# Performance work log

Hardware: AMD Instinct MI355X
Metric: run time of the kernel (lower is better)

The kernel has to match this reference:

```python
import jax, jax.numpy as jnp
import numpy as np
import math

H = 16
D_MODEL = 1024
D_K = D_MODEL // H
MAX_REL = 32
B, S = 2, 2048


def setup_inputs() -> dict:
    key = jax.random.key(0)
    ks = jax.random.split(key, 12)
    def w(k):
        return jax.random.normal(k, (D_MODEL, D_MODEL), jnp.float32) * 0.02
    def b(k):
        return jax.random.normal(k, (D_MODEL,), jnp.float32) * 0.02
    return {
        "query": jax.random.normal(ks[0], (B, S, D_MODEL), jnp.float32),
        "key": jax.random.normal(ks[1], (B, S, D_MODEL), jnp.float32),
        "value": jax.random.normal(ks[2], (B, S, D_MODEL), jnp.float32),
        "mask": jax.random.randint(ks[3], (B, S, S), 0, 2, jnp.int32),
        "Wq": w(ks[4]), "bq": b(ks[5]),
        "Wk": w(ks[6]), "bk": b(ks[7]),
        "Wv": w(ks[8]), "bv": b(ks[9]),
        "Wo": w(ks[10]), "bo": b(ks[11]),
        "rel_emb": jax.random.normal(jax.random.fold_in(key, 99), (2 * MAX_REL + 1, D_K), jnp.float32) * 0.02,
    }


def _rel_bias(q_len, k_len, rel_emb):
    # relative positions clamped to [-MAX_REL, MAX_REL], shifted to [0, 2*MAX_REL]
    rel = jnp.arange(q_len)[:, None] - jnp.arange(k_len)[None, :]
    rel = jnp.clip(rel, -MAX_REL, MAX_REL) + MAX_REL
    # embedding lookup then sum over d_k (torch code: permute(2,0,1).sum(0))
    return rel_emb[rel].sum(-1)  # [q_len, k_len], shared across heads/batch


def reference(query, key, value, mask, Wq, bq, Wk, bk, Wv, bv, Wo, bo, rel_emb):
    nb, qlen, _ = query.shape
    klen = key.shape[1]
    def proj(x, W, b):  # torch Linear: x @ W.T + b -> [B, L, H, D_K] -> [B, H, L, D_K]
        return (x @ W.T + b).reshape(nb, -1, H, D_K).transpose(0, 2, 1, 3)
    q = proj(query, Wq, bq)
    k = proj(key, Wk, bk)
    v = proj(value, Wv, bv)
    scores = jnp.einsum('bhqd,bhkd->bhqk', q, k) / math.sqrt(D_K)
    scores = scores + _rel_bias(qlen, klen, rel_emb)[None, None]
    scores = jnp.where(mask[:, None] == 0, -1e9, scores)
    p = jax.nn.softmax(scores, axis=-1)
    out = jnp.einsum('bhqk,bhkd->bhqd', p, v)
    out = out.transpose(0, 2, 1, 3).reshape(nb, -1, H * D_K)
    return out @ Wo.T + bo
```

## Files before the change

kernel.cpp:

```cpp
#include <hip/hip_runtime.h>
#include <hip/hip_bf16.h>
#include <stdint.h>
#include <math.h>

typedef __bf16 bf16;
typedef __attribute__((ext_vector_type(8))) __bf16 bf16x8;
typedef __attribute__((ext_vector_type(4))) float f32x4;

#define MFMA(a, b, c) __builtin_amdgcn_mfma_f32_16x16x32_bf16(a, b, c, 0, 0, 0)

__device__ __forceinline__ bf16x8 cvt8(const float* p) {
  f32x4 a = *(const f32x4*)p;
  f32x4 b = *(const f32x4*)(p + 4);
  bf16x8 o;
  o[0] = (bf16)a[0]; o[1] = (bf16)a[1]; o[2] = (bf16)a[2]; o[3] = (bf16)a[3];
  o[4] = (bf16)b[0]; o[5] = (bf16)b[1]; o[6] = (bf16)b[2]; o[7] = (bf16)b[3];
  return o;
}

__global__ __launch_bounds__(256) void pack_mask(const int* __restrict__ mask,
                                                 unsigned long long* __restrict__ pm,
                                                 int nwords) {
  const int lane = threadIdx.x & 63;
  const int wave = blockIdx.x * (blockDim.x >> 6) + (threadIdx.x >> 6);
  const int nwaves = gridDim.x * (blockDim.x >> 6);
  for (int w = wave; w < nwords; w += nwaves) {
    int m = mask[(size_t)w * 64 + lane];
    unsigned long long bits = __ballot(m != 0);
    if (lane == 0) pm[w] = bits;
  }
}

template <int SPLIT>
__global__ __launch_bounds__(256) void gemm_bt(const float* __restrict__ X,
                                               const float* __restrict__ W,
                                               const float* __restrict__ bias,
                                               void* __restrict__ out_) {
  __shared__ __align__(16) bf16 As[128 * 32];
  __shared__ __align__(16) bf16 Bs[128 * 32];
  const int tid = threadIdx.x, lane = tid & 63, w = tid >> 6;
  const int r16 = lane & 15, g4 = lane >> 4;
  const int m0 = blockIdx.x * 128, n0 = blockIdx.y * 128;

  f32x4 acc[4][4] = {};

  const int ra = tid >> 2;
  const int ca = (tid & 3) << 3;

  for (int k0 = 0; k0 < 1024; k0 += 32) {
    bf16x8 xa0 = cvt8(&X[(size_t)(m0 + ra) * 1024 + k0 + ca]);
    bf16x8 xa1 = cvt8(&X[(size_t)(m0 + 64 + ra) * 1024 + k0 + ca]);
    bf16x8 xb0 = cvt8(&W[(size_t)(n0 + ra) * 1024 + k0 + ca]);
    bf16x8 xb1 = cvt8(&W[(size_t)(n0 + 64 + ra) * 1024 + k0 + ca]);
    __syncthreads();
    *(bf16x8*)&As[ra * 32 + ca] = xa0;
    *(bf16x8*)&As[(ra + 64) * 32 + ca] = xa1;
    *(bf16x8*)&Bs[ra * 32 + ca] = xb0;
    *(bf16x8*)&Bs[(ra + 64) * 32 + ca] = xb1;
    __syncthreads();

    const int wm = (w >> 1) << 6, wn = (w & 1) << 6;
    bf16x8 af[4], bfr[4];
#pragma unroll
    for (int i = 0; i < 4; i++)
      af[i] = *(const bf16x8*)&As[(wm + i * 16 + r16) * 32 + g4 * 8];
#pragma unroll
    for (int j = 0; j < 4; j++)
      bfr[j] = *(const bf16x8*)&Bs[(wn + j * 16 + r16) * 32 + g4 * 8];
#pragma unroll
    for (int i = 0; i < 4; i++)
#pragma unroll
      for (int j = 0; j < 4; j++)
        acc[i][j] = MFMA(af[i], bfr[j], acc[i][j]);
  }

  const int wm = (w >> 1) << 6, wn = (w & 1) << 6;
#pragma unroll
  for (int j = 0; j < 4; j++) {
    const int col = n0 + wn + j * 16 + r16;
    const float bv = bias[col];
#pragma unroll
    for (int i = 0; i < 4; i++) {
      const int row0 = m0 + wm + i * 16 + g4 * 4;
#pragma unroll
      for (int r = 0; r < 4; r++) {
        float v = acc[i][j][r] + bv;
        const int row = row0 + r;
        if (SPLIT) {
          const int bb = row >> 11, s = row & 2047, h = col >> 6, d = col & 63;
          ((bf16*)out_)[((((size_t)bb * 16 + h) * 2048 + s) << 6) + d] = (bf16)v;
        } else {
          ((float*)out_)[(size_t)row * 1024 + col] = v;
        }
      }
    }
  }
}

__global__ __launch_bounds__(256) void attn_fwd(const bf16* __restrict__ Q,
                                                const bf16* __restrict__ Kb,
                                                const bf16* __restrict__ Vb,
                                                const unsigned long long* __restrict__ pm,
                                                const float* __restrict__ rel,
                                                bf16* __restrict__ ao) {
  constexpr int PAD = 72;
  __shared__ __align__(16) bf16 Ks[64 * PAD];
  __shared__ __align__(16) bf16 Vt[64 * PAD];
  __shared__ __align__(16) bf16 Ps[64 * PAD];
  __shared__ float rb[65];

  const int tid = threadIdx.x, lane = tid & 63, w = tid >> 6;
  const int r16 = lane & 15, g4 = lane >> 4;
  const int qt = blockIdx.x;
  const int bh = blockIdx.y;
  const int b = bh >> 4, h = bh & 15;

  const bf16* Qh = Q + (size_t)bh * 2048 * 64;
  const bf16* Kh = Kb + (size_t)bh * 2048 * 64;
  const bf16* Vh = Vb + (size_t)bh * 2048 * 64;

  if (tid < 65) {
    const float* e = rel + tid * 64;
    float s = 0.f;
#pragma unroll
    for (int i = 0; i < 64; i++) s += e[i];
    rb[tid] = s;
  }

  bf16x8 aq[2];
  {
    const int qrow = (qt << 6) + (w << 4) + r16;
    aq[0] = *(const bf16x8*)&Qh[(size_t)qrow * 64 + g4 * 8];
    aq[1] = *(const bf16x8*)&Qh[(size_t)qrow * 64 + 32 + g4 * 8];
  }

  f32x4 acc_o[4] = {};
  float mreg[4] = {-1e30f, -1e30f, -1e30f, -1e30f};
  float lreg[4] = {0.f, 0.f, 0.f, 0.f};

  __syncthreads();

  for (int t = 0; t < 32; t++) {
#pragma unroll
    for (int cc = 0; cc < 2; cc++) {
      const int c = tid + (cc << 8);
      const int key = c >> 3, f8 = (c & 7) << 3;
      bf16x8 kv = *(const bf16x8*)&Kh[(size_t)((t << 6) + key) * 64 + f8];
      *(bf16x8*)&Ks[key * PAD + f8] = kv;
      bf16x8 vv = *(const bf16x8*)&Vh[(size_t)((t << 6) + key) * 64 + f8];
#pragma unroll
      for (int j = 0; j < 8; j++) Vt[(f8 + j) * PAD + key] = vv[j];
    }
    __syncthreads();

    f32x4 sc[4];
#pragma unroll
    for (int f = 0; f < 4; f++) {
      f32x4 a = {};
#pragma unroll
      for (int kk = 0; kk < 2; kk++) {
        bf16x8 bk_ = *(const bf16x8*)&Ks[(f * 16 + r16) * PAD + kk * 32 + g4 * 8];
        a = MFMA(aq[kk], bk_, a);
      }
      sc[f] = a;
    }

    unsigned long long mw[4];
    const int qrow0 = (qt << 6) + (w << 4) + (g4 << 2);
#pragma unroll
    for (int r = 0; r < 4; r++)
      mw[r] = pm[(size_t)((b << 11) + qrow0 + r) * 32 + t];

    float s_[4][4];
#pragma unroll
    for (int f = 0; f < 4; f++) {
      const int kcol = (t << 6) + (f << 4) + r16;
#pragma unroll
      for (int r = 0; r < 4; r++) {
        int dd = (qrow0 + r) - kcol;
        dd = dd < -32 ? -32 : (dd > 32 ? 32 : dd);
        const bool on = (mw[r] >> ((f << 4) + r16)) & 1ull;
        float x = on ? sc[f][r] * 0.125f + rb[dd + 32] : -1e9f;
        s_[f][r] = (x == x) ? x : -1e9f;
      }
    }

    float rs[4];
#pragma unroll
    for (int r = 0; r < 4; r++) {
      float v = fmaxf(fmaxf(s_[0][r], s_[1][r]), fmaxf(s_[2][r], s_[3][r]));
#pragma unroll
      for (int d = 1; d < 16; d <<= 1) v = fmaxf(v, __shfl_xor(v, d, 16));
      const float mn = fmaxf(mreg[r], v);
      rs[r] = __expf(mreg[r] - mn);
      mreg[r] = mn;
    }
    float ps_[4] = {0.f, 0.f, 0.f, 0.f};
#pragma unroll
    for (int f = 0; f < 4; f++)
#pragma unroll
      for (int r = 0; r < 4; r++) {
        const float p = __expf(s_[f][r] - mreg[r]);
        ps_[r] += p;
        Ps[(w * 16 + g4 * 4 + r) * PAD + f * 16 + r16] = (bf16)p;
      }
#pragma unroll
    for (int r = 0; r < 4; r++) {
      float v = ps_[r];
#pragma unroll
      for (int d = 1; d < 16; d <<= 1) v += __shfl_xor(v, d, 16);
      lreg[r] = lreg[r] * rs[r] + v;
    }
#pragma unroll
    for (int f = 0; f < 4; f++)
#pragma unroll
      for (int r = 0; r < 4; r++) acc_o[f][r] *= rs[r];

#pragma unroll
    for (int kk = 0; kk < 2; kk++) {
      bf16x8 ap = *(const bf16x8*)&Ps[(w * 16 + r16) * PAD + kk * 32 + g4 * 8];
#pragma unroll
      for (int f = 0; f < 4; f++) {
        const int d = f * 16 + r16;
        bf16x8 bv_ = *(const bf16x8*)&Vt[d * PAD + kk * 32 + g4 * 8];
        acc_o[f] = MFMA(ap, bv_, acc_o[f]);
      }
    }
    __syncthreads();
  }

  const int qrow0 = (qt << 6) + (w << 4) + (g4 << 2);
#pragma unroll
  for (int r = 0; r < 4; r++) {
    const float inv = 1.f / lreg[r];
#pragma unroll
    for (int f = 0; f < 4; f++) {
      float v = acc_o[f][r] * inv;
      ao[(size_t)((b << 11) + qrow0 + r) * 1024 + (h << 6) + f * 16 + r16] = (bf16)v;
    }
  }
}

__global__ __launch_bounds__(256) void gemm_out(const bf16* __restrict__ X,
                                                const float* __restrict__ W,
                                                const float* __restrict__ bias,
                                                float* __restrict__ out) {
  __shared__ __align__(16) bf16 As[128 * 32];
  __shared__ __align__(16) bf16 Bs[128 * 32];
  const int tid = threadIdx.x, lane = tid & 63, w = tid >> 6;
  const int r16 = lane & 15, g4 = lane >> 4;
  const int m0 = blockIdx.x * 128, n0 = blockIdx.y * 128;

  f32x4 acc[4][4] = {};
  const int ra = tid >> 2;
  const int ca = (tid & 3) << 3;

  for (int k0 = 0; k0 < 1024; k0 += 32) {
    bf16x8 xa0 = *(const bf16x8*)&X[(size_t)(m0 + ra) * 1024 + k0 + ca];
    bf16x8 xa1 = *(const bf16x8*)&X[(size_t)(m0 + 64 + ra) * 1024 + k0 + ca];
    bf16x8 xb0 = cvt8(&W[(size_t)(n0 + ra) * 1024 + k0 + ca]);
    bf16x8 xb1 = cvt8(&W[(size_t)(n0 + 64 + ra) * 1024 + k0 + ca]);
    __syncthreads();
    *(bf16x8*)&As[ra * 32 + ca] = xa0;
    *(bf16x8*)&As[(ra + 64) * 32 + ca] = xa1;
    *(bf16x8*)&Bs[ra * 32 + ca] = xb0;
    *(bf16x8*)&Bs[(ra + 64) * 32 + ca] = xb1;
    __syncthreads();

    const int wm = (w >> 1) << 6, wn = (w & 1) << 6;
    bf16x8 af[4], bfr[4];
#pragma unroll
    for (int i = 0; i < 4; i++)
      af[i] = *(const bf16x8*)&As[(wm + i * 16 + r16) * 32 + g4 * 8];
#pragma unroll
    for (int j = 0; j < 4; j++)
      bfr[j] = *(const bf16x8*)&Bs[(wn + j * 16 + r16) * 32 + g4 * 8];
#pragma unroll
    for (int i = 0; i < 4; i++)
#pragma unroll
      for (int j = 0; j < 4; j++)
        acc[i][j] = MFMA(af[i], bfr[j], acc[i][j]);
  }

  const int wm = (w >> 1) << 6, wn = (w & 1) << 6;
#pragma unroll
  for (int j = 0; j < 4; j++) {
    const int col = n0 + wn + j * 16 + r16;
    const float bv = bias[col];
#pragma unroll
    for (int i = 0; i < 4; i++) {
      const int row0 = m0 + wm + i * 16 + g4 * 4;
#pragma unroll
      for (int r = 0; r < 4; r++)
        out[(size_t)(row0 + r) * 1024 + col] = acc[i][j][r] + bv;
    }
  }
}

extern "C" void kernel_launch(void* const* d_in, const int* in_sizes, int n_in,
                              void* d_out, int out_size, void* d_ws, size_t ws_size,
                              hipStream_t stream) {
  const float* query = (const float*)d_in[0];
  const float* key   = (const float*)d_in[1];
  const float* value = (const float*)d_in[2];
  const int*   mask  = (const int*)d_in[3];
  const float* Wq = (const float*)d_in[4];
  const float* bq = (const float*)d_in[5];
  const float* Wk = (const float*)d_in[6];
  const float* bk = (const float*)d_in[7];
  const float* Wv = (const float*)d_in[8];
  const float* bv = (const float*)d_in[9];
  const float* Wo = (const float*)d_in[10];
  const float* bo = (const float*)d_in[11];
  const float* rel = (const float*)d_in[12];

  char* ws = (char*)d_ws;
  bf16* Qb = (bf16*)ws;
  bf16* Kb = (bf16*)(ws + 8388608);
  bf16* Vb = (bf16*)(ws + 16777216);
  bf16* AO = (bf16*)(ws + 25165824);
  unsigned long long* PM = (unsigned long long*)(ws + 33554432);

  pack_mask<<<256, 256, 0, stream>>>(mask, PM, 2 * 2048 * 32);

  dim3 g(32, 8);
  gemm_bt<1><<<g, 256, 0, stream>>>(query, Wq, bq, Qb);
  gemm_bt<1><<<g, 256, 0, stream>>>(key,   Wk, bk, Kb);
  gemm_bt<1><<<g, 256, 0, stream>>>(value, Wv, bv, Vb);

  attn_fwd<<<dim3(32, 32), 256, 0, stream>>>(Qb, Kb, Vb, PM, rel, AO);

  gemm_out<<<g, 256, 0, stream>>>(AO, Wo, bo, (float*)d_out);
}
```

Measured before the change: 554.3 us.

## Pre-convert inputs to bf16, prefetch GEMM and attention tiles, swizzle V smem

Adds a kernel that converts the activations and weights to bf16 once, so the GEMMs load bf16 directly. The GEMM tile shrinks to 128x64, which doubles the grid, and each GEMM now prefetches the next K tile into registers during the MFMAs. The attention kernel software-pipelines the K/V loads into registers, stores V in an XOR-swizzled layout instead of a padded transpose, and drops the NaN check. The separate output GEMM is replaced by the generic template. The trade-off is an extra conversion pass over global memory and more workspace.

```diff
diff --git a/kernel.cpp b/kernel.cpp
--- a/kernel.cpp
+++ b/kernel.cpp
@@ -16,6 +16,27 @@
   o[0] = (bf16)a[0]; o[1] = (bf16)a[1]; o[2] = (bf16)a[2]; o[3] = (bf16)a[3];
   o[4] = (bf16)b[0]; o[5] = (bf16)b[1]; o[6] = (bf16)b[2]; o[7] = (bf16)b[3];
   return o;
+}
+
+__global__ __launch_bounds__(256) void cvt_bf16(
+    const float* __restrict__ s0, const float* __restrict__ s1, const float* __restrict__ s2,
+    const float* __restrict__ s3, const float* __restrict__ s4, const float* __restrict__ s5,
+    const float* __restrict__ s6,
+    bf16* __restrict__ d0, bf16* __restrict__ d1, bf16* __restrict__ d2,
+    bf16* __restrict__ d3, bf16* __restrict__ d4, bf16* __restrict__ d5,
+    bf16* __restrict__ d6) {
+  const float* s; bf16* d; int n8;
+  switch (blockIdx.y) {
+    case 0: s = s0; d = d0; n8 = 524288; break;
+    case 1: s = s1; d = d1; n8 = 524288; break;
+    case 2: s = s2; d = d2; n8 = 524288; break;
+    case 3: s = s3; d = d3; n8 = 131072; break;
+    case 4: s = s4; d = d4; n8 = 131072; break;
+    case 5: s = s5; d = d5; n8 = 131072; break;
+    default: s = s6; d = d6; n8 = 131072; break;
+  }
+  for (int i = blockIdx.x * 256 + threadIdx.x; i < n8; i += gridDim.x * 256)
+    *(bf16x8*)&d[(size_t)i * 8] = cvt8(&s[(size_t)i * 8]);
 }
 
 __global__ __launch_bounds__(256) void pack_mask(const int* __restrict__ mask,
@@ -31,52 +52,61 @@
   }
 }
 
-template <int SPLIT>
-__global__ __launch_bounds__(256) void gemm_bt(const float* __restrict__ X,
-                                               const float* __restrict__ W,
+template <int OUT>
+__global__ __launch_bounds__(256) void gemm_bt(const bf16* __restrict__ X,
+                                               const bf16* __restrict__ W,
                                                const float* __restrict__ bias,
                                                void* __restrict__ out_) {
   __shared__ __align__(16) bf16 As[128 * 32];
-  __shared__ __align__(16) bf16 Bs[128 * 32];
+  __shared__ __align__(16) bf16 Bs[64 * 32];
   const int tid = threadIdx.x, lane = tid & 63, w = tid >> 6;
   const int r16 = lane & 15, g4 = lane >> 4;
-  const int m0 = blockIdx.x * 128, n0 = blockIdx.y * 128;
-
-  f32x4 acc[4][4] = {};
+  const int m0 = blockIdx.x * 128, n0 = blockIdx.y * 64;
+
+  f32x4 acc[4][2] = {};
 
   const int ra = tid >> 2;
   const int ca = (tid & 3) << 3;
 
+  bf16x8 xa0 = *(const bf16x8*)&X[(size_t)(m0 + ra) * 1024 + ca];
+  bf16x8 xa1 = *(const bf16x8*)&X[(size_t)(m0 + 64 + ra) * 1024 + ca];
+  bf16x8 xb0 = *(const bf16x8*)&W[(size_t)(n0 + ra) * 1024 + ca];
+  *(bf16x8*)&As[ra * 32 + ca] = xa0;
+  *(bf16x8*)&As[(ra + 64) * 32 + ca] = xa1;
+  *(bf16x8*)&Bs[ra * 32 + ca] = xb0;
+  __syncthreads();
+
+  const int wm = (w >> 1) << 6, wn = (w & 1) << 5;
+
   for (int k0 = 0; k0 < 1024; k0 += 32) {
-    bf16x8 xa0 = cvt8(&X[(size_t)(m0 + ra) * 1024 + k0 + ca]);
-    bf16x8 xa1 = cvt8(&X[(size_t)(m0 + 64 + ra) * 1024 + k0 + ca]);
-    bf16x8 xb0 = cvt8(&W[(size_t)(n0 + ra) * 1024 + k0 + ca]);
-    bf16x8 xb1 = cvt8(&W[(size_t)(n0 + 64 + ra) * 1024 + k0 + ca]);
-    __syncthreads();
-    *(bf16x8*)&As[ra * 32 + ca] = xa0;
-    *(bf16x8*)&As[(ra + 64) * 32 + ca] = xa1;
-    *(bf16x8*)&Bs[ra * 32 + ca] = xb0;
-    *(bf16x8*)&Bs[(ra + 64) * 32 + ca] = xb1;
-    __syncthreads();
-
-    const int wm = (w >> 1) << 6, wn = (w & 1) << 6;
-    bf16x8 af[4], bfr[4];
+    if (k0 + 32 < 1024) {
+      xa0 = *(const bf16x8*)&X[(size_t)(m0 + ra) * 1024 + k0 + 32 + ca];
+      xa1 = *(const bf16x8*)&X[(size_t)(m0 + 64 + ra) * 1024 + k0 + 32 + ca];
+      xb0 = *(const bf16x8*)&W[(size_t)(n0 + ra) * 1024 + k0 + 32 + ca];
+    }
+    bf16x8 af[4], bfr[2];
 #pragma unroll
     for (int i = 0; i < 4; i++)
       af[i] = *(const bf16x8*)&As[(wm + i * 16 + r16) * 32 + g4 * 8];
 #pragma unroll
-    for (int j = 0; j < 4; j++)
+    for (int j = 0; j < 2; j++)
       bfr[j] = *(const bf16x8*)&Bs[(wn + j * 16 + r16) * 32 + g4 * 8];
 #pragma unroll
     for (int i = 0; i < 4; i++)
 #pragma unroll
-      for (int j = 0; j < 4; j++)
+      for (int j = 0; j < 2; j++)
         acc[i][j] = MFMA(af[i], bfr[j], acc[i][j]);
-  }
-
-  const int wm = (w >> 1) << 6, wn = (w & 1) << 6;
-#pragma unroll
-  for (int j = 0; j < 4; j++) {
+    __syncthreads();
+    if (k0 + 32 < 1024) {
+      *(bf16x8*)&As[ra * 32 + ca] = xa0;
+      *(bf16x8*)&As[(ra + 64) * 32 + ca] = xa1;
+      *(bf16x8*)&Bs[ra * 32 + ca] = xb0;
+      __syncthreads();
+    }
+  }
+
+#pragma unroll
+  for (int j = 0; j < 2; j++) {
     const int col = n0 + wn + j * 16 + r16;
     const float bv = bias[col];
 #pragma unroll
@@ -86,7 +116,7 @@
       for (int r = 0; r < 4; r++) {
         float v = acc[i][j][r] + bv;
         const int row = row0 + r;
-        if (SPLIT) {
+        if (OUT) {
           const int bb = row >> 11, s = row & 2047, h = col >> 6, d = col & 63;
           ((bf16*)out_)[((((size_t)bb * 16 + h) * 2048 + s) << 6) + d] = (bf16)v;
         } else {
@@ -105,7 +135,7 @@
                                                 bf16* __restrict__ ao) {
   constexpr int PAD = 72;
   __shared__ __align__(16) bf16 Ks[64 * PAD];
-  __shared__ __align__(16) bf16 Vt[64 * PAD];
+  __shared__ __align__(16) bf16 Vs[64 * 64];
   __shared__ __align__(16) bf16 Ps[64 * PAD];
   __shared__ float rb[65];
 
@@ -138,20 +168,42 @@
   float mreg[4] = {-1e30f, -1e30f, -1e30f, -1e30f};
   float lreg[4] = {0.f, 0.f, 0.f, 0.f};
 
+  int skey[2], sf8[2], svcol[2];
+#pragma unroll
+  for (int cc = 0; cc < 2; cc++) {
+    const int c = tid + (cc << 8);
+    skey[cc] = c >> 3;
+    sf8[cc] = (c & 7) << 3;
+    svcol[cc] = (((skey[cc] >> 3) ^ (c & 7)) << 3) | (skey[cc] & 7);
+  }
+
+  bf16x8 kreg[2], vreg[2];
+#pragma unroll
+  for (int cc = 0; cc < 2; cc++) {
+    kreg[cc] = *(const bf16x8*)&Kh[(size_t)skey[cc] * 64 + sf8[cc]];
+    vreg[cc] = *(const bf16x8*)&Vh[(size_t)skey[cc] * 64 + sf8[cc]];
+  }
+#pragma unroll
+  for (int cc = 0; cc < 2; cc++) {
+    *(bf16x8*)&Ks[skey[cc] * PAD + sf8[cc]] = kreg[cc];
+#pragma unroll
+    for (int j = 0; j < 8; j++) Vs[((sf8[cc] + j) << 6) | svcol[cc]] = vreg[cc][j];
+  }
   __syncthreads();
 
   for (int t = 0; t < 32; t++) {
-#pragma unroll
-    for (int cc = 0; cc < 2; cc++) {
-      const int c = tid + (cc << 8);
-      const int key = c >> 3, f8 = (c & 7) << 3;
-      bf16x8 kv = *(const bf16x8*)&Kh[(size_t)((t << 6) + key) * 64 + f8];
-      *(bf16x8*)&Ks[key * PAD + f8] = kv;
-      bf16x8 vv = *(const bf16x8*)&Vh[(size_t)((t << 6) + key) * 64 + f8];
-#pragma unroll
-      for (int j = 0; j < 8; j++) Vt[(f8 + j) * PAD + key] = vv[j];
-    }
-    __syncthreads();
+    if (t < 31) {
+#pragma unroll
+      for (int cc = 0; cc < 2; cc++) {
+        kreg[cc] = *(const bf16x8*)&Kh[(size_t)(((t + 1) << 6) + skey[cc]) * 64 + sf8[cc]];
+        vreg[cc] = *(const bf16x8*)&Vh[(size_t)(((t + 1) << 6) + skey[cc]) * 64 + sf8[cc]];
+      }
+    }
+    unsigned long long mw[4];
+    const int qrow0 = (qt << 6) + (w << 4) + (g4 << 2);
+#pragma unroll
+    for (int r = 0; r < 4; r++)
+      mw[r] = pm[(size_t)((b << 11) + qrow0 + r) * 32 + t];
 
     f32x4 sc[4];
 #pragma unroll
@@ -164,12 +216,6 @@
       }
       sc[f] = a;
     }
-
-    unsigned long long mw[4];
-    const int qrow0 = (qt << 6) + (w << 4) + (g4 << 2);
-#pragma unroll
-    for (int r = 0; r < 4; r++)
-      mw[r] = pm[(size_t)((b << 11) + qrow0 + r) * 32 + t];
 
     float s_[4][4];
 #pragma unroll
@@ -180,8 +226,7 @@
         int dd = (qrow0 + r) - kcol;
         dd = dd < -32 ? -32 : (dd > 32 ? 32 : dd);
         const bool on = (mw[r] >> ((f << 4) + r16)) & 1ull;
-        float x = on ? sc[f][r] * 0.125f + rb[dd + 32] : -1e9f;
-        s_[f][r] = (x == x) ? x : -1e9f;
+        s_[f][r] = on ? sc[f][r] * 0.125f + rb[dd + 32] : -1e9f;
       }
     }
 
@@ -222,11 +267,20 @@
 #pragma unroll
       for (int f = 0; f < 4; f++) {
         const int d = f * 16 + r16;
-        bf16x8 bv_ = *(const bf16x8*)&Vt[d * PAD + kk * 32 + g4 * 8];
+        bf16x8 bv_ = *(const bf16x8*)&Vs[(d << 6) | ((((kk << 2) + g4) ^ (d >> 3)) << 3)];
         acc_o[f] = MFMA(ap, bv_, acc_o[f]);
       }
     }
     __syncthreads();
+    if (t < 31) {
+#pragma unroll
+      for (int cc = 0; cc < 2; cc++) {
+        *(bf16x8*)&Ks[skey[cc] * PAD + sf8[cc]] = kreg[cc];
+#pragma unroll
+        for (int j = 0; j < 8; j++) Vs[((sf8[cc] + j) << 6) | svcol[cc]] = vreg[cc][j];
+      }
+      __syncthreads();
+    }
   }
 
   const int qrow0 = (qt << 6) + (w << 4) + (g4 << 2);
@@ -237,62 +291,6 @@
     for (int f = 0; f < 4; f++) {
       float v = acc_o[f][r] * inv;
       ao[(size_t)((b << 11) + qrow0 + r) * 1024 + (h << 6) + f * 16 + r16] = (bf16)v;
-    }
-  }
-}
-
-__global__ __launch_bounds__(256) void gemm_out(const bf16* __restrict__ X,
-                                                const float* __restrict__ W,
-                                                const float* __restrict__ bias,
-                                                float* __restrict__ out) {
-  __shared__ __align__(16) bf16 As[128 * 32];
-  __shared__ __align__(16) bf16 Bs[128 * 32];
-  const int tid = threadIdx.x, lane = tid & 63, w = tid >> 6;
-  const int r16 = lane & 15, g4 = lane >> 4;
-  const int m0 = blockIdx.x * 128, n0 = blockIdx.y * 128;
-
-  f32x4 acc[4][4] = {};
-  const int ra = tid >> 2;
-  const int ca = (tid & 3) << 3;
-
-  for (int k0 = 0; k0 < 1024; k0 += 32) {
-    bf16x8 xa0 = *(const bf16x8*)&X[(size_t)(m0 + ra) * 1024 + k0 + ca];
-    bf16x8 xa1 = *(const bf16x8*)&X[(size_t)(m0 + 64 + ra) * 1024 + k0 + ca];
-    bf16x8 xb0 = cvt8(&W[(size_t)(n0 + ra) * 1024 + k0 + ca]);
-    bf16x8 xb1 = cvt8(&W[(size_t)(n0 + 64 + ra) * 1024 + k0 + ca]);
-    __syncthreads();
-    *(bf16x8*)&As[ra * 32 + ca] = xa0;
-    *(bf16x8*)&As[(ra + 64) * 32 + ca] = xa1;
-    *(bf16x8*)&Bs[ra * 32 + ca] = xb0;
-    *(bf16x8*)&Bs[(ra + 64) * 32 + ca] = xb1;
-    __syncthreads();
-
-    const int wm = (w >> 1) << 6, wn = (w & 1) << 6;
-    bf16x8 af[4], bfr[4];
-#pragma unroll
-    for (int i = 0; i < 4; i++)
-      af[i] = *(const bf16x8*)&As[(wm + i * 16 + r16) * 32 + g4 * 8];
-#pragma unroll
-    for (int j = 0; j < 4; j++)
-      bfr[j] = *(const bf16x8*)&Bs[(wn + j * 16 + r16) * 32 + g4 * 8];
-#pragma unroll
-    for (int i = 0; i < 4; i++)
-#pragma unroll
-      for (int j = 0; j < 4; j++)
-        acc[i][j] = MFMA(af[i], bfr[j], acc[i][j]);
-  }
-
-  const int wm = (w >> 1) << 6, wn = (w & 1) << 6;
-#pragma unroll
-  for (int j = 0; j < 4; j++) {
-    const int col = n0 + wn + j * 16 + r16;
-    const float bv = bias[col];
-#pragma unroll
-    for (int i = 0; i < 4; i++) {
-      const int row0 = m0 + wm + i * 16 + g4 * 4;
-#pragma unroll
-      for (int r = 0; r < 4; r++)
-        out[(size_t)(row0 + r) * 1024 + col] = acc[i][j][r] + bv;
     }
   }
 }
@@ -320,15 +318,24 @@
   bf16* Vb = (bf16*)(ws + 16777216);
   bf16* AO = (bf16*)(ws + 25165824);
   unsigned long long* PM = (unsigned long long*)(ws + 33554432);
-
+  bf16* qc  = (bf16*)(ws + 34603008);
+  bf16* kc  = (bf16*)(ws + 42991616);
+  bf16* vc  = (bf16*)(ws + 51380224);
+  bf16* wqc = (bf16*)(ws + 59768832);
+  bf16* wkc = (bf16*)(ws + 61865984);
+  bf16* wvc = (bf16*)(ws + 63963136);
+  bf16* woc = (bf16*)(ws + 66060288);
+
+  cvt_bf16<<<dim3(256, 7), 256, 0, stream>>>(query, key, value, Wq, Wk, Wv, Wo,
+                                             qc, kc, vc, wqc, wkc, wvc, woc);
   pack_mask<<<256, 256, 0, stream>>>(mask, PM, 2 * 2048 * 32);
 
-  dim3 g(32, 8);
-  gemm_bt<1><<<g, 256, 0, stream>>>(query, Wq, bq, Qb);
-  gemm_bt<1><<<g, 256, 0, stream>>>(key,   Wk, bk, Kb);
-  gemm_bt<1><<<g, 256, 0, stream>>>(value, Wv, bv, Vb);
+  dim3 g(32, 16);
+  gemm_bt<1><<<g, 256, 0, stream>>>(qc, wqc, bq, Qb);
+  gemm_bt<1><<<g, 256, 0, stream>>>(kc, wkc, bk, Kb);
+  gemm_bt<1><<<g, 256, 0, stream>>>(vc, wvc, bv, Vb);
 
   attn_fwd<<<dim3(32, 32), 256, 0, stream>>>(Qb, Kb, Vb, PM, rel, AO);
 
-  gemm_out<<<g, 256, 0, stream>>>(AO, Wo, bo, (float*)d_out);
-}
+  gemm_bt<0><<<g, 256, 0, stream>>>(AO, woc, bo, (float*)d_out);
+}
```

Result: faster. 458.3 us (-17.3%).
